# Optimization experiments

Hardware: AMD Instinct MI355X
Metric: run time of the kernel (lower is better)

Reference implementation:

```python
import jax, jax.numpy as jnp
import numpy as np

B, T, S, H, V, E = 32, 256, 32, 512, 128, 512


def setup_inputs() -> dict:
    key = jax.random.key(0)
    ks = jax.random.split(key, 20)
    f = lambda i, shape: jax.random.normal(ks[i], shape, jnp.float32) * 0.05
    return dict(
        embedding=f(0, (V, H)),
        scope_enc=f(1, (B, S, H)),
        spec_enc=f(2, (B, E)),
        W_init=f(3, (H, E)), b_init=jnp.zeros((H,), jnp.float32),
        W_ih=f(4, (3 * H, 2 * H)), W_hh=f(5, (3 * H, H)),
        b_ih=jnp.zeros((3 * H,), jnp.float32), b_hh=jnp.zeros((3 * H,), jnp.float32),
        W_out=f(6, (V, H)), b_out=jnp.zeros((V,), jnp.float32),
        Wd=f(7, (H, H)), We=f(8, (H, H)), v_attn=f(9, (H,)),
        tokens_in=jax.random.randint(ks[10], (B, T), 0, V),
        tokens_out=jax.random.randint(ks[11], (B, T), 0, V),
        pointer_ids=jax.random.randint(ks[12], (B, T), 0, S),
        ptr_targets=jax.random.randint(ks[13], (B, T), 0, S),
        pointer_mask=jax.random.bernoulli(ks[14], 0.25, (B, T)),
    )


def _gru(x_proj, h0, W_hh, b_hh):
    # x_proj: [B,T,3H] precomputed input projection; torch GRU gate order (r,z,n)
    def step(h, xp):
        gh = h @ W_hh.T + b_hh
        xr, xz, xn = jnp.split(xp, 3, axis=-1)
        hr, hz, hn = jnp.split(gh, 3, axis=-1)
        r = jax.nn.sigmoid(xr + hr)
        z = jax.nn.sigmoid(xz + hz)
        n = jnp.tanh(xn + r * hn)
        h_new = (1.0 - z) * n + z * h
        return h_new, h_new
    _, outs = jax.lax.scan(step, h0, jnp.swapaxes(x_proj, 0, 1))
    return jnp.swapaxes(outs, 0, 1)  # [B,T,H]


def reference(embedding, scope_enc, spec_enc, W_init, b_init, W_ih, W_hh, b_ih, b_hh,
              W_out, b_out, Wd, We, v_attn,
              tokens_in, tokens_out, pointer_ids, ptr_targets, pointer_mask):
    h0 = spec_enc @ W_init.T + b_init                      # initialState
    x_emb = embedding[tokens_in]                           # [B,T,H]
    obj = jax.vmap(lambda s, i: s[i])(scope_enc, pointer_ids)  # [B,T,H]
    obj = jnp.where(pointer_mask[:, :, None], obj, 0.0)    # objectInputs (zeros for non-pointers)
    x = jnp.concatenate([x_emb, obj], axis=-1)             # [B,T,2H]
    x_proj = x @ W_ih.T + b_ih                             # [B,T,3H]
    o = _gru(x_proj, h0, W_hh, b_hh)                       # decoder states [B,T,H]

    # token log-likelihood: -nll_loss(log_softmax(output(o)), targets), summed
    logp = jax.nn.log_softmax(o @ W_out.T + b_out, axis=-1)
    tok_ll = jnp.take_along_axis(logp, tokens_out[:, :, None], axis=-1)[..., 0].sum(-1)

    # pointer attention: additive attention with tanh, log_softmax over scope
    hd = o @ Wd.T                                          # decoderToPointer [B,T,H]
    ok = scope_enc @ We.T                                  # encoderToPointer [B,S,H]
    att = jnp.tanh(hd[:, :, None, :] + ok[:, None, :, :]) @ v_attn  # [B,T,S]
    logatt = jax.nn.log_softmax(att, axis=-1)
    ptr_ll = jnp.take_along_axis(logatt, ptr_targets[:, :, None], axis=-1)[..., 0]
    ptr_ll = jnp.where(pointer_mask, ptr_ll, 0.0).sum(-1)

    return tok_ll + ptr_ll  # per-program likelihood [B]
```

## Files before the change

### kernel.cpp

```cpp
#include <hip/hip_runtime.h>
#include <stdint.h>

#define NB 32
#define NT 256
#define NS 32
#define NH 512
#define NV 128
#define BT 8192

typedef __attribute__((ext_vector_type(8))) __bf16 bf16x8;
typedef __attribute__((ext_vector_type(4))) float f32x4;
typedef __attribute__((ext_vector_type(2))) _Float16 half2v;
typedef unsigned long long u64;

typedef __attribute__((address_space(1))) const unsigned int GASU;
typedef __attribute__((address_space(3))) unsigned int LASU;
#define ASYNC16(g, l) __builtin_amdgcn_global_load_lds((GASU*)(g), (LASU*)(l), 16, 0, 0)

__device__ __forceinline__ half2v pkrtz(float a, float b){
  return __builtin_bit_cast(half2v, __builtin_amdgcn_cvt_pkrtz(a, b));
}
__device__ __forceinline__ unsigned short f2bf(float f){
  unsigned int u = __builtin_bit_cast(unsigned int, f);
  u += 0x7fffu + ((u >> 16) & 1u);
  return (unsigned short)(u >> 16);
}
__device__ __forceinline__ float bf2f(unsigned short h){
  return __builtin_bit_cast(float, ((unsigned int)h) << 16);
}
__device__ __forceinline__ float fexp(float x){ return __builtin_amdgcn_exp2f(x * 1.4426950408889634f); }
__device__ __forceinline__ float fsigm(float x){ return __builtin_amdgcn_rcpf(1.f + fexp(-x)); }
__device__ __forceinline__ float ftanh(float x){
  float t = __builtin_amdgcn_exp2f(x * 2.8853900817779268f);
  return (t - 1.f) * __builtin_amdgcn_rcpf(t + 1.f);
}
__device__ __forceinline__ float flog(float x){ return __builtin_amdgcn_logf(x) * 0.6931471805599453f; }

__device__ __forceinline__ u64 ld_l2(const u64* p){
  u64 v;
  asm volatile("global_load_dwordx2 %0, %1, off sc0\n\ts_waitcnt vmcnt(0)"
               : "=v"(v) : "v"(p) : "memory");
  return v;
}
__device__ __forceinline__ void st_l2(u64* p, u64 v){
  asm volatile("global_store_dwordx2 %0, %1, off" :: "v"(p), "v"(v) : "memory");
}

__global__ void k_prep(const float* __restrict__ emb, const float* __restrict__ scope,
                       const float* __restrict__ Wih, const float* __restrict__ Wout,
                       const float* __restrict__ Wd,  const float* __restrict__ We,
                       unsigned short* e_o, unsigned short* s_o, unsigned short* wi_o,
                       unsigned short* wo_o, unsigned short* wd_o, unsigned short* we_o,
                       u64* hx, u64* hxL, float* out, unsigned short* zbuf){
  int g = blockIdx.x*256 + threadIdx.x, gs = gridDim.x*256;
  if (g < 2*NB*256){
    hx[g] = 0ull;
    __hip_atomic_store(hxL + g, 0ull, __ATOMIC_RELAXED, __HIP_MEMORY_SCOPE_AGENT);
  }
  if (g < NB) out[g] = 0.f;
  if (g < 2048) zbuf[g] = 0;
  for (int i=g; i<NV*NH;      i+=gs) e_o[i]  = f2bf(emb[i]);
  for (int i=g; i<NB*NS*NH;   i+=gs) s_o[i]  = f2bf(scope[i]);
  for (int i=g; i<3*NH*2*NH;  i+=gs) wi_o[i] = f2bf(Wih[i]);
  for (int i=g; i<NV*NH;      i+=gs) wo_o[i] = f2bf(Wout[i]);
  for (int i=g; i<NH*NH;      i+=gs) wd_o[i] = f2bf(Wd[i]);
  for (int i=g; i<NH*NH;      i+=gs) we_o[i] = f2bf(We[i]);
}

__global__ void k_h0(const float* __restrict__ spec, const float* __restrict__ Winit,
                     const float* __restrict__ binit, float* __restrict__ h032,
                     u64* __restrict__ hx, u64* __restrict__ hxL){
  const int b = blockIdx.x, tid = threadIdx.x, lane = tid & 63, w = tid >> 6;
  __shared__ float sp[NH];
  __shared__ float hres[NH];
  if (tid < 128) *(float4*)&sp[tid*4] = *(const float4*)(spec + b*NH + tid*4);
  __syncthreads();
  for (int i = 0; i < 128; ++i){
    int j = w * 128 + i;
    const float4* wr = (const float4*)(Winit + (size_t)j * NH);
    float4 x0 = wr[lane*2], x1 = wr[lane*2 + 1];
    float p = x0.x*sp[lane*8]   + x0.y*sp[lane*8+1] + x0.z*sp[lane*8+2] + x0.w*sp[lane*8+3]
            + x1.x*sp[lane*8+4] + x1.y*sp[lane*8+5] + x1.z*sp[lane*8+6] + x1.w*sp[lane*8+7];
    #pragma unroll
    for (int o = 1; o < 64; o <<= 1) p += __shfl_xor(p, o);
    if (lane == 0){
      float v = p + binit[j];
      h032[b*NH + j] = v;
      hres[j] = v;
    }
  }
  __syncthreads();
  if (tid < 256){
    unsigned int pw = __builtin_bit_cast(unsigned int, pkrtz(hres[2*tid], hres[2*tid+1]));
    u64 pv = (1ull << 32) | (u64)pw;
    __hip_atomic_store(hx + b*256 + tid, pv, __ATOMIC_RELAXED, __HIP_MEMORY_SCOPE_AGENT);
    __hip_atomic_store(hxL + b*256 + tid, pv, __ATOMIC_RELAXED, __HIP_MEMORY_SCOPE_AGENT);
  }
}

struct GatherArgs {
  const int* tok; const int* pid; const int* msk;
  const unsigned short* emb; const unsigned short* scope; const unsigned short* zbuf;
};

template<int ASRC>
__global__ __launch_bounds__(256, 2) void k_gemm(
    const unsigned short* __restrict__ A, const unsigned short* __restrict__ Bw,
    float* __restrict__ Cf, unsigned short* __restrict__ Cbf,
    const float* __restrict__ bias, int M, int N, int K, GatherArgs ga)
{
  __shared__ unsigned short lA[2][128][64];
  __shared__ unsigned short lB[2][128][64];
  const int tid = threadIdx.x, lane = tid & 63, wv = tid >> 6;
  const int m0 = blockIdx.x * 128, n0 = blockIdx.y * 128;

  const unsigned short* srcA[4];
  const unsigned short* srcO[4];
  const unsigned short* srcB[4];
  #pragma unroll
  for (int i = 0; i < 4; ++i){
    int ar = m0 + wv*32 + i*8 + (lane >> 3);
    int chunk = (lane & 7) * 8;
    if (ASRC == 0){
      srcA[i] = A + (size_t)ar * K + chunk;
      srcO[i] = nullptr;
    } else {
      int tk = ga.tok[ar], pd = ga.pid[ar], mk = ga.msk[ar];
      srcA[i] = ga.emb + (size_t)tk * NH + chunk;
      srcO[i] = mk ? (ga.scope + ((size_t)((ar >> 8) * NS + pd)) * NH + chunk)
                   : (ga.zbuf + chunk);
    }
    int br = n0 + wv*32 + i*8 + (lane >> 3);
    srcB[i] = Bw + (size_t)br * K + chunk;
  }

  f32x4 acc[4][4];
  #pragma unroll
  for (int x=0;x<4;++x)
    #pragma unroll
    for (int y=0;y<4;++y) acc[x][y] = (f32x4){0.f,0.f,0.f,0.f};

  auto STAGE = [&](int bf, int kt){
    const int k0 = kt * 64;
    #pragma unroll
    for (int i = 0; i < 4; ++i){
      const unsigned short* pa;
      if (ASRC == 0) pa = srcA[i] + k0;
      else pa = (k0 < NH) ? (srcA[i] + k0) : (srcO[i] + (k0 - NH));
      ASYNC16(pa, &lA[bf][wv*32 + i*8][0]);
      ASYNC16(srcB[i] + k0, &lB[bf][wv*32 + i*8][0]);
    }
  };

  STAGE(0, 0);
  asm volatile("s_waitcnt vmcnt(0)" ::: "memory");
  __syncthreads();

  const int wm = (wv >> 1) * 64, wn = (wv & 1) * 64;
  const int fr = lane & 15, fq = lane >> 4;
  const int nt = K >> 6;
  int cur = 0;
  for (int kt = 0; kt < nt; ++kt){
    if (kt + 1 < nt) STAGE(cur ^ 1, kt + 1);
    #pragma unroll
    for (int ks = 0; ks < 2; ++ks){
      bf16x8 af[4], bfv[4];
      #pragma unroll
      for (int mi = 0; mi < 4; ++mi)
        af[mi] = *(const bf16x8*)&lA[cur][wm + mi*16 + fr][ks*32 + fq*8];
      #pragma unroll
      for (int ni = 0; ni < 4; ++ni)
        bfv[ni] = *(const bf16x8*)&lB[cur][wn + ni*16 + fr][ks*32 + fq*8];
      #pragma unroll
      for (int mi = 0; mi < 4; ++mi)
        #pragma unroll
        for (int ni = 0; ni < 4; ++ni)
          acc[mi][ni] = __builtin_amdgcn_mfma_f32_16x16x32_bf16(af[mi], bfv[ni], acc[mi][ni], 0, 0, 0);
    }
    asm volatile("s_waitcnt vmcnt(0)" ::: "memory");
    __syncthreads();
    cur ^= 1;
  }

  #pragma unroll
  for (int mi = 0; mi < 4; ++mi){
    #pragma unroll
    for (int ni = 0; ni < 4; ++ni){
      int col = n0 + wn + ni*16 + fr;
      float bv = bias ? bias[col] : 0.f;
      #pragma unroll
      for (int rr = 0; rr < 4; ++rr){
        int row = m0 + wm + mi*16 + fq*4 + rr;
        float v = acc[mi][ni][rr] + bv;
        if (Cbf) Cbf[(size_t)row * N + col] = f2bf(v);
        else     Cf [(size_t)row * N + col] = v;
      }
    }
  }
}

__global__ __launch_bounds__(512, 1) void k_gru(
    const float* __restrict__ Whh, const float* __restrict__ bhh,
    const unsigned short* __restrict__ xp,
    const float* __restrict__ h032,
    u64* __restrict__ hx,
    u64* __restrict__ hxL,
    unsigned short* __restrict__ obf)
{
  const int bid = blockIdx.x;
  const int b = bid & 31, s = bid >> 5;
  const int tid = threadIdx.x;
  const int u = tid >> 3, r = tid & 7;
  const int jg = s * 64 + u;

  __shared__ __align__(16) unsigned int hl[256];
  __shared__ float xpl[192];
  __shared__ unsigned int pkb[32];

  half2v w0[8][4], w1[8][4], w2[8][4];
  #pragma unroll
  for (int c = 0; c < 8; ++c){
    const int kb = r*64 + ((c + r) & 7) * 8;
    const float* p0 = Whh + ((size_t)(       jg)) * NH + kb;
    const float* p1 = Whh + ((size_t)(  NH + jg)) * NH + kb;
    const float* p2 = Whh + ((size_t)(2*NH + jg)) * NH + kb;
    #pragma unroll
    for (int p = 0; p < 4; ++p){
      float2 a = *(const float2*)(p0 + 2*p);
      float2 c2 = *(const float2*)(p1 + 2*p);
      float2 d = *(const float2*)(p2 + 2*p);
      w0[c][p] = pkrtz(a.x, a.y);
      w1[c][p] = pkrtz(c2.x, c2.y);
      w2[c][p] = pkrtz(d.x, d.y);
    }
  }
  const float bh0 = bhh[jg], bh1 = bhh[NH + jg], bh2 = bhh[2*NH + jg];
  float hprev = h032[b*NH + jg];

  unsigned short xpv = 0;
  if (tid >= 256 && tid < 448){
    int idx = tid - 256;
    xpv = xp[((size_t)(b*NT + 0)) * 1536 + (idx >> 6) * NH + s*64 + (idx & 63)];
  }

  for (int t = 0; t < NT; ++t){
    if (tid < 256){
      const int base = (((t & 1) * NB + b) << 8) + tid;
      u64 v;
      while (true){
        v = ld_l2(hxL + base);
        if ((unsigned int)(v >> 32) == (unsigned int)(t + 1)) break;
        v = __hip_atomic_load(hx + base, __ATOMIC_RELAXED,
                              __HIP_MEMORY_SCOPE_AGENT);
        if ((unsigned int)(v >> 32) == (unsigned int)(t + 1)) break;
      }
      hl[tid] = (unsigned int)v;
    } else if (tid < 448){
      int idx = tid - 256;
      xpl[idx] = bf2f(xpv);
      if (t + 1 < NT)
        xpv = xp[((size_t)(b*NT + t + 1)) * 1536 + (idx >> 6) * NH + s*64 + (idx & 63)];
    }
    __syncthreads();

    float a0 = 0.f, a1 = 0.f, a2 = 0.f;
    half2v hch[8][4];
    #pragma unroll
    for (int c = 0; c < 8; ++c){
      const int g = (r << 3) + ((c + r) & 7);
      uint4 hv = *(const uint4*)&hl[g * 4];
      hch[c][0] = __builtin_bit_cast(half2v, hv.x);
      hch[c][1] = __builtin_bit_cast(half2v, hv.y);
      hch[c][2] = __builtin_bit_cast(half2v, hv.z);
      hch[c][3] = __builtin_bit_cast(half2v, hv.w);
    }
    #pragma unroll
    for (int c = 0; c < 8; ++c){
      #pragma unroll
      for (int p = 0; p < 4; ++p){
        a0 = __builtin_amdgcn_fdot2(w0[c][p], hch[c][p], a0, false);
        a1 = __builtin_amdgcn_fdot2(w1[c][p], hch[c][p], a1, false);
        a2 = __builtin_amdgcn_fdot2(w2[c][p], hch[c][p], a2, false);
      }
    }
    a0 += __shfl_xor(a0, 1); a0 += __shfl_xor(a0, 2); a0 += __shfl_xor(a0, 4);
    a1 += __shfl_xor(a1, 1); a1 += __shfl_xor(a1, 2); a1 += __shfl_xor(a1, 4);
    a2 += __shfl_xor(a2, 1); a2 += __shfl_xor(a2, 2); a2 += __shfl_xor(a2, 4);

    float hnew = 0.f;
    if (r == 0){
      float xr = xpl[u], xz = xpl[64 + u], xn = xpl[128 + u];
      float rg = fsigm(xr + a0 + bh0);
      float zg = fsigm(xz + a1 + bh1);
      float ng = ftanh(xn + rg * (a2 + bh2));
      hnew = (1.f - zg) * ng + zg * hprev;
      hprev = hnew;
    }
    float hpart = __shfl_xor(hnew, 8);
    if (r == 0 && (u & 1) == 0){
      unsigned int pw = __builtin_bit_cast(unsigned int, pkrtz(hnew, hpart));
      u64 pv = ((u64)(unsigned int)(t + 2) << 32) | (u64)pw;
      const int dst = ((((t + 1) & 1) * NB + b) << 8) + (s << 5) + (u >> 1);
      st_l2(hxL + dst, pv);
      __hip_atomic_store(hx + dst, pv,
                         __ATOMIC_RELAXED, __HIP_MEMORY_SCOPE_AGENT);
      pkb[u >> 1] = (unsigned int)f2bf(hnew) | ((unsigned int)f2bf(hpart) << 16);
    }
    __syncthreads();

    if (tid >= 448 && tid < 480){
      int i = tid - 448;
      ((unsigned int*)obf)[((size_t)(b*NT + t)) * (NH/2) + s*32 + i] = pkb[i];
    }
  }
}

__global__ void k_tokll(const float* __restrict__ logits, const int* __restrict__ tko,
                        float* __restrict__ out){
  const int tid = threadIdx.x, lane = tid & 63, w = tid >> 6;
  const int r0 = blockIdx.x * 64 + w * 16;
  const int b = r0 >> 8;
  int mytok = 0; float tval = 0.f;
  if (lane < 16){
    mytok = tko[r0 + lane];
    tval = logits[(size_t)(r0 + lane) * NV + mytok];
  }
  float acc = 0.f;
  for (int i = 0; i < 16; ++i){
    const float* L = logits + (size_t)(r0 + i) * NV;
    float l0 = L[lane], l1 = L[64 + lane];
    float m = fmaxf(l0, l1);
    #pragma unroll
    for (int o = 1; o < 64; o <<= 1) m = fmaxf(m, __shfl_xor(m, o));
    float sm = fexp(l0 - m) + fexp(l1 - m);
    #pragma unroll
    for (int o = 1; o < 64; o <<= 1) sm += __shfl_xor(sm, o);
    float lse = m + flog(sm);
    float tv = __shfl(tval, i);
    if (lane == 0) acc += tv - lse;
  }
  if (lane == 0) atomicAdd(out + b, acc);
}

__global__ __launch_bounds__(256, 2) void k_ptr(
    const unsigned short* __restrict__ hd, const float* __restrict__ okp,
    const float* __restrict__ vat, const int* __restrict__ ptg,
    const int* __restrict__ pmask, float* __restrict__ out)
{
  __shared__ unsigned short okl[NS][518];
  __shared__ unsigned short hdl[16][518];
  __shared__ float vl[NH];
  __shared__ float attl[16][33];
  const int tid = threadIdx.x;
  const int b = blockIdx.x >> 4, t0 = (blockIdx.x & 15) * 16;
  for (int ii = 0; ii < 64; ++ii){
    int lin = ii*256 + tid;
    int s = lin >> 9, h = lin & 511;
    okl[s][h] = f2bf(okp[((size_t)(b*NS + s)) * NH + h]);
  }
  for (int ii = 0; ii < 32; ++ii){
    int lin = ii*256 + tid;
    int tt = lin >> 9, h = lin & 511;
    hdl[tt][h] = hd[((size_t)(b*NT + t0 + tt)) * NH + h];
  }
  vl[tid] = vat[tid]; vl[256 + tid] = vat[256 + tid];
  __syncthreads();
  #pragma unroll
  for (int pp = 0; pp < 2; ++pp){
    int p = pp*256 + tid;
    int tt = p >> 5, s = p & 31;
    float a = 0.f;
    #pragma unroll 4
    for (int h = 0; h < NH; ++h)
      a += vl[h] * ftanh(bf2f(hdl[tt][h]) + bf2f(okl[s][h]));
    attl[tt][s] = a;
  }
  __syncthreads();
  if (tid < 16){
    int tt = tid;
    float m = -1e30f;
    for (int s = 0; s < NS; ++s) m = fmaxf(m, attl[tt][s]);
    float sm = 0.f;
    for (int s = 0; s < NS; ++s) sm += fexp(attl[tt][s] - m);
    float lse = m + flog(sm);
    int g = b*NT + t0 + tt;
    float c = pmask[g] ? (attl[tt][ptg[g]] - lse) : 0.f;
    #pragma unroll
    for (int o = 1; o < 16; o <<= 1) c += __shfl_xor(c, o);
    if (tid == 0) atomicAdd(out + b, c);
  }
}

extern "C" void kernel_launch(void* const* d_in, const int* in_sizes, int n_in,
                              void* d_out, int out_size, void* d_ws, size_t ws_size,
                              hipStream_t stream)
{
  (void)in_sizes; (void)n_in; (void)out_size; (void)ws_size;
  const float* embedding  = (const float*)d_in[0];
  const float* scope_enc  = (const float*)d_in[1];
  const float* spec_enc   = (const float*)d_in[2];
  const float* W_init     = (const float*)d_in[3];
  const float* b_init     = (const float*)d_in[4];
  const float* W_ih       = (const float*)d_in[5];
  const float* W_hh       = (const float*)d_in[6];
  const float* b_ih       = (const float*)d_in[7];
  const float* b_hh       = (const float*)d_in[8];
  const float* W_out      = (const float*)d_in[9];
  const float* b_out      = (const float*)d_in[10];
  const float* Wd         = (const float*)d_in[11];
  const float* We         = (const float*)d_in[12];
  const float* v_attn     = (const float*)d_in[13];
  const int* tokens_in    = (const int*)d_in[14];
  const int* tokens_out   = (const int*)d_in[15];
  const int* pointer_ids  = (const int*)d_in[16];
  const int* ptr_targets  = (const int*)d_in[17];
  const int* pointer_mask = (const int*)d_in[18];
  float* outF = (float*)d_out;

  uint8_t* wp = (uint8_t*)d_ws;
  auto carve = [&](size_t bytes)->void*{
    void* p = (void*)wp; wp += (bytes + 255) & ~(size_t)255; return p;
  };
  unsigned short* xp_bf    = (unsigned short*)carve((size_t)BT*1536*2);
  unsigned short* o_bf     = (unsigned short*)carve((size_t)BT*NH*2);
  float*          logitsF  = (float*)carve((size_t)BT*NV*4);
  unsigned short* hd_bf    = (unsigned short*)carve((size_t)BT*NH*2);
  float*          okp      = (float*)carve((size_t)NB*NS*NH*4);
  unsigned short* emb_bf   = (unsigned short*)carve((size_t)NV*NH*2);
  unsigned short* scope_bf = (unsigned short*)carve((size_t)NB*NS*NH*2);
  unsigned short* Wih_bf   = (unsigned short*)carve((size_t)3*NH*2*NH*2);
  unsigned short* Wout_bf  = (unsigned short*)carve((size_t)NV*NH*2);
  unsigned short* Wd_bf    = (unsigned short*)carve((size_t)NH*NH*2);
  unsigned short* We_bf    = (unsigned short*)carve((size_t)NH*NH*2);
  float*          h032     = (float*)carve((size_t)NB*NH*4);
  u64*            hx       = (u64*)carve((size_t)2*NB*256*8);
  u64*            hxL      = (u64*)carve((size_t)2*NB*256*8);
  unsigned short* zbuf     = (unsigned short*)carve(4096);

  hipLaunchKernelGGL(k_prep, dim3(1024), dim3(256), 0, stream,
                     embedding, scope_enc, W_ih, W_out, Wd, We,
                     emb_bf, scope_bf, Wih_bf, Wout_bf, Wd_bf, We_bf,
                     hx, hxL, outF, zbuf);
  hipLaunchKernelGGL(k_h0, dim3(NB), dim3(256), 0, stream, spec_enc, W_init, b_init,
                     h032, hx, hxL);
  GatherArgs ga{tokens_in, pointer_ids, pointer_mask, emb_bf, scope_bf, zbuf};
  GatherArgs g0{nullptr,nullptr,nullptr,nullptr,nullptr,nullptr};
  hipLaunchKernelGGL((k_gemm<1>), dim3(64,12), dim3(256), 0, stream,
                     (const unsigned short*)nullptr, Wih_bf, (float*)nullptr, xp_bf,
                     b_ih, BT, 1536, 1024, ga);
  hipLaunchKernelGGL(k_gru, dim3(256), dim3(512), 0, stream,
                     W_hh, b_hh, xp_bf, h032, hx, hxL, o_bf);
  hipLaunchKernelGGL((k_gemm<0>), dim3(64,1), dim3(256), 0, stream,
                     o_bf, Wout_bf, logitsF, (unsigned short*)nullptr, b_out, BT, NV, NH, g0);
  hipLaunchKernelGGL((k_gemm<0>), dim3(64,4), dim3(256), 0, stream,
                     o_bf, Wd_bf, (float*)nullptr, hd_bf, (const float*)nullptr, BT, NH, NH, g0);
  hipLaunchKernelGGL((k_gemm<0>), dim3(8,4), dim3(256), 0, stream,
                     scope_bf, We_bf, okp, (unsigned short*)nullptr, (const float*)nullptr,
                     NB*NS, NH, NH, g0);
  hipLaunchKernelGGL(k_tokll, dim3(128), dim3(256), 0, stream, logitsF, tokens_out, outF);
  hipLaunchKernelGGL(k_ptr, dim3(512), dim3(256), 0, stream,
                     hd_bf, okp, v_attn, ptr_targets, pointer_mask, outF);
}
```

Before: 675.6 us.

## Assign GRU work slots by XCD so each batch's slices share an L2

Each GRU workgroup reads its hardware XCC id and atomically claims a slot from that XCD's range. All 8 hidden-slice workgroups of the same batch row therefore land on one XCD and exchange hidden state through a shared L2 instead of across dies. The spin-wait also polls the agent-scope fallback only every fourth iteration, which cuts cross-die traffic. In exchange it adds a claim array, an atomic CAS loop at kernel start and an extra barrier, and it assumes the hardware places workgroups evenly across the XCDs.

```diff
diff --git a/kernel.cpp b/kernel.cpp
--- a/kernel.cpp
+++ b/kernel.cpp
@@ -51,12 +51,13 @@
                        const float* __restrict__ Wd,  const float* __restrict__ We,
                        unsigned short* e_o, unsigned short* s_o, unsigned short* wi_o,
                        unsigned short* wo_o, unsigned short* wd_o, unsigned short* we_o,
-                       u64* hx, u64* hxL, float* out, unsigned short* zbuf){
+                       u64* hx, u64* hxL, int* claim, float* out, unsigned short* zbuf){
   int g = blockIdx.x*256 + threadIdx.x, gs = gridDim.x*256;
   if (g < 2*NB*256){
     hx[g] = 0ull;
     __hip_atomic_store(hxL + g, 0ull, __ATOMIC_RELAXED, __HIP_MEMORY_SCOPE_AGENT);
   }
+  if (g < 256) __hip_atomic_store(claim + g, 0, __ATOMIC_RELAXED, __HIP_MEMORY_SCOPE_AGENT);
   if (g < NB) out[g] = 0.f;
   if (g < 2048) zbuf[g] = 0;
   for (int i=g; i<NV*NH;      i+=gs) e_o[i]  = f2bf(emb[i]);
@@ -205,11 +206,26 @@
     const float* __restrict__ h032,
     u64* __restrict__ hx,
     u64* __restrict__ hxL,
+    int* __restrict__ claim,
     unsigned short* __restrict__ obf)
 {
-  const int bid = blockIdx.x;
-  const int b = bid & 31, s = bid >> 5;
   const int tid = threadIdx.x;
+  __shared__ int slotS;
+  if (tid == 0){
+    unsigned int xcd;
+    asm volatile("s_getreg_b32 %0, hwreg(HW_REG_XCC_ID)" : "=s"(xcd));
+    xcd &= 7;
+    int slot = -1;
+    for (int i = 0; i < 256; ++i){
+      int cand = (int)((xcd << 5) + i) & 255;
+      if (atomicCAS(claim + cand, 0, 1) == 0){ slot = cand; break; }
+    }
+    slotS = slot;
+  }
+  __syncthreads();
+  const int slot = slotS;
+  const int b = ((slot >> 5) << 2) + ((slot >> 3) & 3);
+  const int s = slot & 7;
   const int u = tid >> 3, r = tid & 7;
   const int jg = s * 64 + u;
 
@@ -242,17 +258,21 @@
     int idx = tid - 256;
     xpv = xp[((size_t)(b*NT + 0)) * 1536 + (idx >> 6) * NH + s*64 + (idx & 63)];
   }
+  __syncthreads();
 
   for (int t = 0; t < NT; ++t){
     if (tid < 256){
       const int base = (((t & 1) * NB + b) << 8) + tid;
-      u64 v;
+      const unsigned int want = (unsigned int)(t + 1);
+      u64 v; int it = 0;
       while (true){
         v = ld_l2(hxL + base);
-        if ((unsigned int)(v >> 32) == (unsigned int)(t + 1)) break;
-        v = __hip_atomic_load(hx + base, __ATOMIC_RELAXED,
-                              __HIP_MEMORY_SCOPE_AGENT);
-        if ((unsigned int)(v >> 32) == (unsigned int)(t + 1)) break;
+        if ((unsigned int)(v >> 32) == want) break;
+        if ((++it & 3) == 0){
+          v = __hip_atomic_load(hx + base, __ATOMIC_RELAXED,
+                                __HIP_MEMORY_SCOPE_AGENT);
+          if ((unsigned int)(v >> 32) == want) break;
+        }
       }
       hl[tid] = (unsigned int)v;
     } else if (tid < 448){
@@ -435,12 +455,13 @@
   float*          h032     = (float*)carve((size_t)NB*NH*4);
   u64*            hx       = (u64*)carve((size_t)2*NB*256*8);
   u64*            hxL      = (u64*)carve((size_t)2*NB*256*8);
+  int*            claim    = (int*)carve(1024);
   unsigned short* zbuf     = (unsigned short*)carve(4096);
 
   hipLaunchKernelGGL(k_prep, dim3(1024), dim3(256), 0, stream,
                      embedding, scope_enc, W_ih, W_out, Wd, We,
                      emb_bf, scope_bf, Wih_bf, Wout_bf, Wd_bf, We_bf,
-                     hx, hxL, outF, zbuf);
+                     hx, hxL, claim, outF, zbuf);
   hipLaunchKernelGGL(k_h0, dim3(NB), dim3(256), 0, stream, spec_enc, W_init, b_init,
                      h032, hx, hxL);
   GatherArgs ga{tokens_in, pointer_ids, pointer_mask, emb_bf, scope_bf, zbuf};
@@ -449,7 +470,7 @@
                      (const unsigned short*)nullptr, Wih_bf, (float*)nullptr, xp_bf,
                      b_ih, BT, 1536, 1024, ga);
   hipLaunchKernelGGL(k_gru, dim3(256), dim3(512), 0, stream,
-                     W_hh, b_hh, xp_bf, h032, hx, hxL, o_bf);
+                     W_hh, b_hh, xp_bf, h032, hx, hxL, claim, o_bf);
   hipLaunchKernelGGL((k_gemm<0>), dim3(64,1), dim3(256), 0, stream,
                      o_bf, Wout_bf, logitsF, (unsigned short*)nullptr, b_out, BT, NV, NH, g0);
   hipLaunchKernelGGL((k_gemm<0>), dim3(64,4), dim3(256), 0, stream,
```

New measurement: 816.1 us. 20.8% more time.

## Pipeline spin-wait loads and use lightweight LDS-only barriers in GRU recurrence

Applied to the files above, without the earlier changes.

The flag-polling loop in the persistent GRU kernel now keeps two relaxed atomic loads in flight at once, instead of issuing a blocking sc0 load followed by a full vmcnt wait. It checks the fallback mirror buffer only every eighth iteration. The per-step __syncthreads calls are replaced by a custom barrier that waits only on lgkmcnt and then issues s_barrier, so outstanding global stores and prefetch loads are not drained at each step. The goal is lower cross-block synchronization latency on the serial recurrence path. The risk is memory-ordering problems if a global load result is needed across the barrier, and the relaxed atomics may be served from a stale cache.

```diff
diff --git a/kernel.cpp b/kernel.cpp
--- a/kernel.cpp
+++ b/kernel.cpp
@@ -36,15 +36,16 @@
 }
 __device__ __forceinline__ float flog(float x){ return __builtin_amdgcn_logf(x) * 0.6931471805599453f; }
 
-__device__ __forceinline__ u64 ld_l2(const u64* p){
-  u64 v;
-  asm volatile("global_load_dwordx2 %0, %1, off sc0\n\ts_waitcnt vmcnt(0)"
-               : "=v"(v) : "v"(p) : "memory");
-  return v;
-}
 __device__ __forceinline__ void st_l2(u64* p, u64 v){
   asm volatile("global_store_dwordx2 %0, %1, off" :: "v"(p), "v"(v) : "memory");
 }
+
+#define BAR() do{ \
+  asm volatile("s_waitcnt lgkmcnt(0)" ::: "memory"); \
+  __builtin_amdgcn_sched_barrier(0); \
+  __builtin_amdgcn_s_barrier(); \
+  __builtin_amdgcn_sched_barrier(0); \
+}while(0)
 
 __global__ void k_prep(const float* __restrict__ emb, const float* __restrict__ scope,
                        const float* __restrict__ Wih, const float* __restrict__ Wout,
@@ -242,17 +243,26 @@
     int idx = tid - 256;
     xpv = xp[((size_t)(b*NT + 0)) * 1536 + (idx >> 6) * NH + s*64 + (idx & 63)];
   }
+  __syncthreads();
 
   for (int t = 0; t < NT; ++t){
     if (tid < 256){
       const int base = (((t & 1) * NB + b) << 8) + tid;
+      const u64* pL = hxL + base;
+      const u64* pM = hx + base;
+      const unsigned int want = (unsigned int)(t + 1);
       u64 v;
+      u64 a  = __hip_atomic_load(pL, __ATOMIC_RELAXED, __HIP_MEMORY_SCOPE_AGENT);
+      u64 b2 = __hip_atomic_load(pL, __ATOMIC_RELAXED, __HIP_MEMORY_SCOPE_AGENT);
+      int it = 0;
       while (true){
-        v = ld_l2(hxL + base);
-        if ((unsigned int)(v >> 32) == (unsigned int)(t + 1)) break;
-        v = __hip_atomic_load(hx + base, __ATOMIC_RELAXED,
-                              __HIP_MEMORY_SCOPE_AGENT);
-        if ((unsigned int)(v >> 32) == (unsigned int)(t + 1)) break;
+        if ((unsigned int)(a >> 32) == want){ v = a; break; }
+        a = b2;
+        b2 = __hip_atomic_load(pL, __ATOMIC_RELAXED, __HIP_MEMORY_SCOPE_AGENT);
+        if (((++it) & 7) == 0){
+          u64 m = __hip_atomic_load(pM, __ATOMIC_RELAXED, __HIP_MEMORY_SCOPE_AGENT);
+          if ((unsigned int)(m >> 32) == want){ v = m; break; }
+        }
       }
       hl[tid] = (unsigned int)v;
     } else if (tid < 448){
@@ -261,7 +271,7 @@
       if (t + 1 < NT)
         xpv = xp[((size_t)(b*NT + t + 1)) * 1536 + (idx >> 6) * NH + s*64 + (idx & 63)];
     }
-    __syncthreads();
+    BAR();
 
     float a0 = 0.f, a1 = 0.f, a2 = 0.f;
     half2v hch[8][4];
@@ -306,7 +316,7 @@
                          __ATOMIC_RELAXED, __HIP_MEMORY_SCOPE_AGENT);
       pkb[u >> 1] = (unsigned int)f2bf(hnew) | ((unsigned int)f2bf(hpart) << 16);
     }
-    __syncthreads();
+    BAR();
 
     if (tid >= 448 && tid < 480){
       int i = tid - 448;
```

New measurement: 646.0 us. 1.05x faster.
